# Performance work log

Measured on AMD Instinct MI355X. Metric: run time of the kernel, lower is better.

## Reference

```python
import jax, jax.numpy as jnp
import numpy as np

B, SEQ, DIM = 32, 512, 1024
DEPTH, HEADS, DHEAD = 6, 8, 64
INNER = HEADS * DHEAD  # 512
NLAT, MAXSEQ = 64, 512
EPS = 1e-5


def setup_inputs() -> dict:
    key = jax.random.key(0)
    ks = jax.random.split(key, 8)
    return {
        "x": jax.random.normal(ks[0], (B, SEQ, DIM), dtype=jnp.float32),
        "attention_mask": jax.random.randint(ks[1], (B, SEQ), 0, 2, dtype=jnp.int32),
        "latents": jax.random.normal(ks[2], (NLAT, DIM), dtype=jnp.float32),
        "media_pos_emb": jax.random.normal(ks[3], (MAXSEQ, DIM), dtype=jnp.float32),
        "ln_media_g": jnp.ones((DEPTH, DIM), jnp.float32),
        "ln_media_b": jnp.zeros((DEPTH, DIM), jnp.float32),
        "ln_lat_g": jnp.ones((DEPTH, DIM), jnp.float32),
        "ln_lat_b": jnp.zeros((DEPTH, DIM), jnp.float32),
        "Wq": jax.random.normal(ks[4], (DEPTH, DIM, INNER), dtype=jnp.float32) * 0.02,
        "Wkv": jax.random.normal(ks[5], (DEPTH, DIM, 2 * INNER), dtype=jnp.float32) * 0.02,
        "Wout": jax.random.normal(ks[6], (DEPTH, INNER, DIM), dtype=jnp.float32) * 0.02,
        "final_g": jnp.ones((DIM,), jnp.float32),
        "final_b": jnp.zeros((DIM,), jnp.float32),
    }


def _layer_norm(x, g, b):
    mu = jnp.mean(x, axis=-1, keepdims=True)
    var = jnp.mean(jnp.square(x - mu), axis=-1, keepdims=True)
    return (x - mu) * jax.lax.rsqrt(var + EPS) * g + b


def _heads(t):
    # b n (h d) -> b h n d
    b, n, _ = t.shape
    return t.reshape(b, n, HEADS, DHEAD).transpose(0, 2, 1, 3)


def reference(x, attention_mask, latents, media_pos_emb, ln_media_g, ln_media_b,
              ln_lat_g, ln_lat_b, Wq, Wkv, Wout, final_g, final_b):
    b, seq, _ = x.shape
    x = x + media_pos_emb[None, :seq, :]
    lat = jnp.broadcast_to(latents[None], (b, NLAT, DIM))
    scale = DHEAD ** -0.5
    # key mask over [latents ++ media]: latent keys never masked; 1 == masked
    key_mask = jnp.concatenate(
        [jnp.zeros((b, NLAT), attention_mask.dtype), attention_mask], axis=1)
    masked = (key_mask == 1)[:, None, None, :]  # b 1 1 j
    for l in range(DEPTH):
        xm = _layer_norm(x, ln_media_g[l], ln_media_b[l])
        ln = _layer_norm(lat, ln_lat_g[l], ln_lat_b[l])
        q = _heads(ln @ Wq[l])                      # b h i d
        kv = jnp.concatenate([ln, xm], axis=1) @ Wkv[l]
        k, v = jnp.split(kv, 2, axis=-1)
        k, v = _heads(k), _heads(v)                 # b h j d
        sim = jnp.einsum('bhid,bhjd->bhij', q * scale, k)
        sim = jnp.where(masked, -jnp.inf, sim)
        attn = jax.nn.softmax(sim, axis=-1)
        out = jnp.einsum('bhij,bhjd->bhid', attn, v)
        out = out.transpose(0, 2, 1, 3).reshape(b, NLAT, INNER)
        lat = lat + out @ Wout[l]
    return _layer_norm(lat, final_g, final_b)
```

## Files before the change

### kernel.cpp

```cpp
#include <hip/hip_runtime.h>
#include <cstdint>


#define DEVINL __device__ __forceinline__

typedef __attribute__((ext_vector_type(8))) short short8_t;
typedef __attribute__((ext_vector_type(4))) float f32x4;

DEVINL ushort f2bf(float f) {
  union { float f; uint32_t u; } c; c.f = f;
  uint32_t u = c.u;
  u += ((u >> 16) & 1u) + 0x7fffu;
  return (ushort)(u >> 16);
}
DEVINL float bf2f(ushort u) {
  union { uint32_t u; float f; } c; c.u = ((uint32_t)u) << 16;
  return c.f;
}
DEVINL f32x4 mfma16(short8_t a, short8_t b, f32x4 c) {
  return __builtin_amdgcn_mfma_f32_16x16x32_bf16(a, b, c, 0, 0, 0);
}
DEVINL void gld16(ushort* lds, const ushort* g) {
  __builtin_amdgcn_global_load_lds(
      (const __attribute__((address_space(1))) void*)g,
      (__attribute__((address_space(3))) void*)lds, 16, 0, 0);
}

__global__ __launch_bounds__(512, 2) void k_gemm256m(const ushort* __restrict__ A,
    const ushort* __restrict__ Bt, const float* __restrict__ bias,
    ushort* __restrict__ Kb, ushort* __restrict__ Vt) {
  extern __shared__ char lds[];
  constexpr int K = 1024, NT = 16;
  int tid = threadIdx.x, lane = tid & 63, w = tid >> 6;
  int wm = w >> 2, wn = w & 3;
  int fr = lane & 15;
  int fkb = (lane >> 4) << 4;
  int xorv = (fr & 7) << 4;
  int bid = blockIdx.x;
  int xcd = bid & 7, ii = bid >> 3;
  int m0 = (xcd * 8 + (ii >> 2)) * 256;
  int n0 = (ii & 3) * 256;
  int srow = w * 8 + (lane >> 3);
  int sce = ((lane & 7) ^ (lane >> 3)) << 3;
  const ushort* Ag = A + (size_t)(m0 + srow) * K + sce;
  const ushort* Bg = Bt + (size_t)(n0 + srow) * K + sce;
  f32x4 acc[8][4] = {};

  auto stA = [&](int t, int h) {
    ushort* d = (ushort*)(lds + (t % 3) * 32768 + h * 16384 + w * 1024);
    const ushort* s = Ag + (size_t)(h * 128) * K + t * 64;
    gld16(d, s);
    gld16((ushort*)((char*)d + 8192), s + (size_t)64 * K);
  };
  auto stB = [&](int t, int h) {
    ushort* d = (ushort*)(lds + 98304 + (t & 1) * 32768 + h * 16384 + w * 1024);
    const ushort* s = Bg + (size_t)(h * 128) * K + t * 64;
    gld16(d, s);
    gld16((ushort*)((char*)d + 8192), s + (size_t)64 * K);
  };
  stA(0, 0); stA(0, 1); stB(0, 0); stB(0, 1); stA(1, 0); stA(1, 1);

#define RD_AFR(DST, MQ)                                                        \
  _Pragma("unroll") for (int m2 = 0; m2 < 2; ++m2)                             \
    _Pragma("unroll") for (int kh = 0; kh < 2; ++kh)                           \
      DST[m2][kh] = *(const short8_t*)(ab +                                    \
          ((wm * 128 + (MQ + m2) * 16 + fr) << 7) + ((kh * 64 + fkb) ^ xorv));

#define CLUSTER(MQ, AFR)                                                       \
  __builtin_amdgcn_s_setprio(1);                                               \
  _Pragma("unroll") for (int kh = 0; kh < 2; ++kh)                             \
    _Pragma("unroll") for (int m2 = 0; m2 < 2; ++m2)                           \
      _Pragma("unroll") for (int nt = 0; nt < 4; ++nt)                         \
        acc[MQ + m2][nt] = mfma16(AFR[m2][kh], bfr[nt][kh], acc[MQ + m2][nt]); \
  __builtin_amdgcn_s_setprio(0);                                               \
  __builtin_amdgcn_s_barrier();

  for (int t = 0; t < NT; ++t) {
    const char* ab = lds + (t % 3) * 32768;
    const char* bb = lds + 98304 + (t & 1) * 32768;
    short8_t bfr[4][2], afrX[2][2], afrY[2][2];
    if (t + 1 < NT) asm volatile("s_waitcnt vmcnt(4)" ::: "memory");
    else            asm volatile("s_waitcnt vmcnt(0)" ::: "memory");
    __builtin_amdgcn_s_barrier();
#pragma unroll
    for (int nt = 0; nt < 4; ++nt)
#pragma unroll
      for (int kh = 0; kh < 2; ++kh)
        bfr[nt][kh] = *(const short8_t*)(bb +
            ((wn * 64 + nt * 16 + fr) << 7) + ((kh * 64 + fkb) ^ xorv));
    RD_AFR(afrX, 0);
    if (t + 1 < NT) stB(t + 1, 0);
    RD_AFR(afrY, 2);
    CLUSTER(0, afrX);
    if (t + 1 < NT) stB(t + 1, 1);
    RD_AFR(afrX, 4);
    CLUSTER(2, afrY);
    if (t + 2 < NT) stA(t + 2, 0);
    RD_AFR(afrY, 6);
    CLUSTER(4, afrX);
    if (t + 2 < NT) stA(t + 2, 1);
    CLUSTER(6, afrY);
  }
#undef RD_AFR
#undef CLUSTER

  __syncthreads();
  ushort* Cl = (ushort*)lds;
  constexpr int CLS = 264;
  bool isV = (n0 >= 512);
#pragma unroll
  for (int mt = 0; mt < 8; ++mt)
#pragma unroll
    for (int nt = 0; nt < 4; ++nt)
#pragma unroll
      for (int r = 0; r < 4; ++r) {
        int rl = wm * 128 + mt * 16 + ((lane >> 4) << 2) + r;
        int cl = wn * 64 + nt * 16 + fr;
        ushort v = f2bf(acc[mt][nt][r] + bias[n0 + cl]);
        if (!isV) Cl[rl * CLS + cl] = v;
        else      Cl[cl * CLS + rl] = v;
      }
  __syncthreads();
  int b_ = m0 >> 9;
  int jb = 64 + (m0 & 511);
#pragma unroll
  for (int q2 = 0; q2 < 16; ++q2) {
    int task = tid + q2 * 512;
    int rr2 = task >> 5, c8 = task & 31;
    short8_t vv = *(const short8_t*)&Cl[rr2 * CLS + c8 * 8];
    if (!isV)
      *(short8_t*)&Kb[((size_t)(b_ * 576 + jb + rr2) << 9) + n0 + c8 * 8] = vv;
    else
      *(short8_t*)&Vt[(size_t)(b_ * 512 + (n0 - 512) + rr2) * 576 + jb + c8 * 8] = vv;
  }
}

__global__ __launch_bounds__(512) void k_attn(const ushort* __restrict__ Q,
    const ushort* __restrict__ Kb, const ushort* __restrict__ Vt,
    const int* __restrict__ amask, ushort* __restrict__ AO) {
  extern __shared__ char alds[];
  ushort* sim = (ushort*)alds;
  char* stg = alds + 74752;
  int bh = blockIdx.x;
  int h = bh & 7, b = bh >> 3;
  int tid = threadIdx.x, lane = tid & 63, w = tid >> 6;
  int rg = w >> 1, ch = w & 1;
  int fr = lane & 15;
  int fkb = (lane >> 4) << 4;
  int csrc8 = ((lane & 7) ^ (lane >> 3)) << 3;
  short8_t aq0, aq1;
  {
    int qi = rg * 16 + fr;
    const ushort* qp = Q + ((size_t)(b * 64 + qi) << 9) + h * 64 + ((lane >> 4) << 3);
    aq0 = *(const short8_t*)qp;
    aq1 = *(const short8_t*)(qp + 32);
  }
  unsigned mbits = 0;
#pragma unroll
  for (int c = 1; c < 9; ++c)
    if (amask[b * 512 + (c - 1) * 64 + lane]) mbits |= (1u << c);

  auto stageK = [&](int it, int buf) {
#pragma unroll
    for (int g = 0; g < 3; ++g) {
      int sr = w * 24 + g * 8 + (lane >> 3);
      ushort* d = (ushort*)(stg + buf * 24576 + (w * 24 + g * 8) * 128);
      gld16(d, Kb + ((size_t)(b * 576 + it * 192 + sr) << 9) + h * 64 + csrc8);
    }
  };
  auto stageV = [&](int it, int buf) {
#pragma unroll
    for (int g = 0; g < 3; ++g) {
      int sr = w * 8 + (lane >> 3);
      ushort* d = (ushort*)(stg + buf * 24576 + g * 8192 + w * 8 * 128);
      gld16(d, Vt + (size_t)(b * 512 + h * 64 + sr) * 576 + it * 192 + g * 64 + csrc8);
    }
  };

  stageK(0, 0);
  for (int it = 0; it < 3; ++it) {
    int buf = it & 1;
    __builtin_amdgcn_s_barrier();
    if (it + 1 < 3) {
      stageK(it + 1, buf ^ 1);
      asm volatile("s_waitcnt vmcnt(3)" ::: "memory");
    } else {
      asm volatile("s_waitcnt vmcnt(0)" ::: "memory");
    }
    __builtin_amdgcn_s_barrier();
    const char* kb_ = stg + buf * 24576;
#pragma unroll
    for (int ct = 0; ct < 6; ++ct) {
      int row_l = ch * 96 + ct * 16 + fr;
      const char* base = kb_ + row_l * 128;
      int sw = (row_l & 7) << 4;
      short8_t k0 = *(const short8_t*)(base + (fkb ^ sw));
      short8_t k1 = *(const short8_t*)(base + ((64 + fkb) ^ sw));
      f32x4 s4 = {};
      s4 = mfma16(aq0, k0, s4);
      s4 = mfma16(aq1, k1, s4);
#pragma unroll
      for (int r = 0; r < 4; ++r)
        sim[(rg * 16 + ((lane >> 4) << 2) + r) * 584 +
            it * 192 + ch * 96 + ct * 16 + fr] = f2bf(s4[r]);
    }
  }
  __syncthreads();
  for (int rr = 0; rr < 8; ++rr) {
    int row = w * 8 + rr;
    float vals[9];
    float m = -3.0e38f;
#pragma unroll
    for (int c = 0; c < 9; ++c) {
      float v = bf2f(sim[row * 584 + c * 64 + lane]);
      vals[c] = v;
      if (!((mbits >> c) & 1)) m = fmaxf(m, v);
    }
#pragma unroll
    for (int off = 32; off; off >>= 1) m = fmaxf(m, __shfl_xor(m, off));
    float ssum = 0.f;
    float p[9];
#pragma unroll
    for (int c = 0; c < 9; ++c) {
      p[c] = ((mbits >> c) & 1) ? 0.f : __expf(vals[c] - m);
      ssum += p[c];
    }
#pragma unroll
    for (int off = 32; off; off >>= 1) ssum += __shfl_xor(ssum, off);
    float inv = 1.0f / ssum;
#pragma unroll
    for (int c = 0; c < 9; ++c)
      sim[row * 584 + c * 64 + lane] = f2bf(p[c] * inv);
  }
  __syncthreads();
  f32x4 oacc[2] = {};
  stageV(0, 0);
  for (int it = 0; it < 3; ++it) {
    int buf = it & 1;
    __builtin_amdgcn_s_barrier();
    if (it + 1 < 3) {
      stageV(it + 1, buf ^ 1);
      asm volatile("s_waitcnt vmcnt(3)" ::: "memory");
    } else {
      asm volatile("s_waitcnt vmcnt(0)" ::: "memory");
    }
    __builtin_amdgcn_s_barrier();
#pragma unroll
    for (int g = 0; g < 3; ++g) {
      const char* vb_ = stg + buf * 24576 + g * 8192;
      const ushort* srow_ = &sim[(rg * 16 + fr) * 584 + it * 192 + g * 64];
      short8_t pa0 = *(const short8_t*)(srow_ + ((lane >> 4) << 3));
      short8_t pa1 = *(const short8_t*)(srow_ + 32 + ((lane >> 4) << 3));
#pragma unroll
      for (int dt = 0; dt < 2; ++dt) {
        int row_l = ch * 32 + dt * 16 + fr;
        const char* base = vb_ + row_l * 128;
        int sw = (row_l & 7) << 4;
        short8_t v0 = *(const short8_t*)(base + (fkb ^ sw));
        short8_t v1 = *(const short8_t*)(base + ((64 + fkb) ^ sw));
        oacc[dt] = mfma16(pa0, v0, oacc[dt]);
        oacc[dt] = mfma16(pa1, v1, oacc[dt]);
      }
    }
  }
#pragma unroll
  for (int dt = 0; dt < 2; ++dt)
#pragma unroll
    for (int r = 0; r < 4; ++r) {
      int i = rg * 16 + ((lane >> 4) << 2) + r;
      int d = ch * 32 + dt * 16 + fr;
      AO[((size_t)(b * 64 + i) << 9) + h * 64 + d] = f2bf(oacc[dt][r]);
    }
}

__global__ __launch_bounds__(256) void k_fold_kv(const float* __restrict__ Wkv,
    const float* __restrict__ lnmg, const float* __restrict__ lnlg,
    const float* __restrict__ lnmb, const float* __restrict__ lnlb,
    ushort* __restrict__ wkvmT, ushort* __restrict__ wlatT,
    float* __restrict__ bkvm, float* __restrict__ blat) {
  __shared__ float tile[32][33];
  __shared__ float pm[8][32], pl[8][32];
  int l = blockIdx.y;
  int c0 = blockIdx.x * 32;
  const float* Wl = Wkv + (size_t)l * 1048576;
  int tx = threadIdx.x & 31, ty = threadIdx.x >> 5;
  float am = 0.f, al = 0.f;
  for (int rt = 0; rt < 32; ++rt) {
    int r0 = rt * 32;
    __syncthreads();
#pragma unroll
    for (int i = 0; i < 4; ++i)
      tile[ty + i * 8][tx] = Wl[(size_t)(r0 + ty + i * 8) * 1024 + c0 + tx];
    __syncthreads();
#pragma unroll
    for (int i = 0; i < 4; ++i) {
      int r = ty * 4 + i;
      float wv = tile[r][tx];
      am += lnmb[l * 1024 + r0 + r] * wv;
      al += lnlb[l * 1024 + r0 + r] * wv;
    }
#pragma unroll
    for (int i = 0; i < 4; ++i) {
      int c = ty + i * 8;
      float wv = tile[tx][c];
      int r = r0 + tx;
      wkvmT[(size_t)l * 1048576 + (size_t)(c0 + c) * 1024 + r] =
          f2bf(wv * lnmg[l * 1024 + r]);
      wlatT[(size_t)l * 1572864 + (size_t)(512 + c0 + c) * 1024 + r] =
          f2bf(wv * lnlg[l * 1024 + r]);
    }
  }
  pm[ty][tx] = am; pl[ty][tx] = al;
  __syncthreads();
  if (ty == 0) {
    float sm = 0.f, sl = 0.f;
#pragma unroll
    for (int k = 0; k < 8; ++k) { sm += pm[k][tx]; sl += pl[k][tx]; }
    bkvm[l * 1024 + c0 + tx] = sm;
    blat[l * 1536 + 512 + c0 + tx] = sl;
  }
}

__global__ __launch_bounds__(256) void k_fold_q(const float* __restrict__ Wq,
    const float* __restrict__ lnlg, const float* __restrict__ lnlb,
    ushort* __restrict__ wlatT, float* __restrict__ blat) {
  __shared__ float tile[32][33];
  __shared__ float pq[8][32];
  int l = blockIdx.y;
  int c0 = blockIdx.x * 32;
  const float* Wl = Wq + (size_t)l * 524288;
  int tx = threadIdx.x & 31, ty = threadIdx.x >> 5;
  float aq = 0.f;
  for (int rt = 0; rt < 32; ++rt) {
    int r0 = rt * 32;
    __syncthreads();
#pragma unroll
    for (int i = 0; i < 4; ++i)
      tile[ty + i * 8][tx] = Wl[(size_t)(r0 + ty + i * 8) * 512 + c0 + tx];
    __syncthreads();
#pragma unroll
    for (int i = 0; i < 4; ++i) {
      int r = ty * 4 + i;
      aq += lnlb[l * 1024 + r0 + r] * tile[r][tx];
    }
#pragma unroll
    for (int i = 0; i < 4; ++i) {
      int c = ty + i * 8;
      float wv = tile[tx][c];
      int r = r0 + tx;
      wlatT[(size_t)l * 1572864 + (size_t)(c0 + c) * 1024 + r] =
          f2bf(wv * lnlg[l * 1024 + r] * 0.125f);
    }
  }
  pq[ty][tx] = aq;
  __syncthreads();
  if (ty == 0) {
    float s = 0.f;
#pragma unroll
    for (int k = 0; k < 8; ++k) s += pq[k][tx];
    blat[l * 1536 + c0 + tx] = s * 0.125f;
  }
}

__global__ __launch_bounds__(256) void k_fold_out(const float* __restrict__ Wout,
    ushort* __restrict__ woutT) {
  __shared__ float tile[32][33];
  int l = blockIdx.z;
  const float* Wl = Wout + (size_t)l * 524288;
  int r0 = blockIdx.y * 32, c0 = blockIdx.x * 32;
  int tx = threadIdx.x & 31, ty = threadIdx.x >> 5;
#pragma unroll
  for (int i = 0; i < 4; ++i)
    tile[ty + i * 8][tx] = Wl[(size_t)(r0 + ty + i * 8) * 1024 + c0 + tx];
  __syncthreads();
#pragma unroll
  for (int i = 0; i < 4; ++i) {
    int jl = ty + i * 8;
    woutT[(size_t)l * 524288 + (size_t)(c0 + jl) * 512 + r0 + tx] = f2bf(tile[tx][jl]);
  }
}

__global__ __launch_bounds__(256) void k_rownorm(const float* __restrict__ in,
    const float* __restrict__ pos, ushort* __restrict__ out) {
  int row = blockIdx.x, t = threadIdx.x;
  float4 v = *(const float4*)(in + (size_t)row * 1024 + t * 4);
  if (pos) {
    float4 p = *(const float4*)(pos + (size_t)(row & 511) * 1024 + t * 4);
    v.x += p.x; v.y += p.y; v.z += p.z; v.w += p.w;
  }
  float s = v.x + v.y + v.z + v.w;
  float q = v.x * v.x + v.y * v.y + v.z * v.z + v.w * v.w;
#pragma unroll
  for (int off = 32; off; off >>= 1) { s += __shfl_xor(s, off); q += __shfl_xor(q, off); }
  __shared__ float rs[4], rq[4];
  if ((t & 63) == 0) { rs[t >> 6] = s; rq[t >> 6] = q; }
  __syncthreads();
  s = rs[0] + rs[1] + rs[2] + rs[3];
  q = rq[0] + rq[1] + rq[2] + rq[3];
  float mean = s * (1.0f / 1024.0f);
  float var = q * (1.0f / 1024.0f) - mean * mean;
  float rstd = rsqrtf(var + 1e-5f);
  ushort4 o;
  o.x = f2bf((v.x - mean) * rstd);
  o.y = f2bf((v.y - mean) * rstd);
  o.z = f2bf((v.z - mean) * rstd);
  o.w = f2bf((v.w - mean) * rstd);
  *(ushort4*)(out + (size_t)row * 1024 + t * 4) = o;
}

__global__ __launch_bounds__(256) void k_finalln(const float* __restrict__ in,
    const float* __restrict__ g, const float* __restrict__ b, float* __restrict__ out) {
  int row = blockIdx.x, t = threadIdx.x;
  float4 v = *(const float4*)(in + (size_t)row * 1024 + t * 4);
  float s = v.x + v.y + v.z + v.w;
  float q = v.x * v.x + v.y * v.y + v.z * v.z + v.w * v.w;
#pragma unroll
  for (int off = 32; off; off >>= 1) { s += __shfl_xor(s, off); q += __shfl_xor(q, off); }
  __shared__ float rs[4], rq[4];
  if ((t & 63) == 0) { rs[t >> 6] = s; rq[t >> 6] = q; }
  __syncthreads();
  s = rs[0] + rs[1] + rs[2] + rs[3];
  q = rq[0] + rq[1] + rq[2] + rq[3];
  float mean = s * (1.0f / 1024.0f);
  float var = q * (1.0f / 1024.0f) - mean * mean;
  float rstd = rsqrtf(var + 1e-5f);
  float4 g4 = *(const float4*)(g + t * 4);
  float4 b4 = *(const float4*)(b + t * 4);
  float4 o;
  o.x = (v.x - mean) * rstd * g4.x + b4.x;
  o.y = (v.y - mean) * rstd * g4.y + b4.y;
  o.z = (v.z - mean) * rstd * g4.z + b4.z;
  o.w = (v.w - mean) * rstd * g4.w + b4.w;
  *(float4*)(out + (size_t)row * 1024 + t * 4) = o;
}

__global__ __launch_bounds__(256) void k_latinit(const float* __restrict__ latents,
                                                 float* __restrict__ lat) {
  int row = blockIdx.x, t = threadIdx.x;
  *(float4*)(lat + (size_t)row * 1024 + t * 4) =
      *(const float4*)(latents + (size_t)(row & 63) * 1024 + t * 4);
}

template <int MODE>
__global__ __launch_bounds__(256) void k_gemm64(const ushort* __restrict__ A,
    const ushort* __restrict__ Bt, const float* __restrict__ bias,
    ushort* __restrict__ o0, ushort* __restrict__ o1, ushort* __restrict__ o2,
    float* __restrict__ of, int N, int K) {
  __shared__ ushort Al[2][64][32];
  __shared__ ushort Bl[2][64][32];
  __shared__ ushort Cl[64][72];
  int tid = threadIdx.x, lane = tid & 63, w = tid >> 6;
  int wr = w >> 1, wc = w & 1;
  int m0 = blockIdx.y * 64, n0 = blockIdx.x * 64;
  f32x4 acc[2][2] = {};
  const ushort* Ag = A + (size_t)(m0 + w * 16 + (lane >> 2)) * K + (lane & 3) * 8;
  const ushort* Bg = Bt + (size_t)(n0 + w * 16 + (lane >> 2)) * K + (lane & 3) * 8;
  int fr = lane & 15, fk = (lane >> 4) << 3;
  int nt = K >> 5;
  gld16(&Al[0][w * 16][0], Ag);
  gld16(&Bl[0][w * 16][0], Bg);
  __syncthreads();
  for (int t = 0; t < nt; ++t) {
    int cur = t & 1;
    if (t + 1 < nt) {
      int k0 = (t + 1) << 5;
      gld16(&Al[cur ^ 1][w * 16][0], Ag + k0);
      gld16(&Bl[cur ^ 1][w * 16][0], Bg + k0);
    }
    short8_t a[2], b[2];
#pragma unroll
    for (int mt = 0; mt < 2; ++mt)
      a[mt] = *(const short8_t*)&Al[cur][wr * 32 + mt * 16 + fr][fk];
#pragma unroll
    for (int nt2 = 0; nt2 < 2; ++nt2)
      b[nt2] = *(const short8_t*)&Bl[cur][wc * 32 + nt2 * 16 + fr][fk];
#pragma unroll
    for (int mt = 0; mt < 2; ++mt)
#pragma unroll
      for (int nt2 = 0; nt2 < 2; ++nt2)
        acc[mt][nt2] = mfma16(a[mt], b[nt2], acc[mt][nt2]);
    __syncthreads();
  }
  if constexpr (MODE == 3) {
    if (n0 >= 1024) {
#pragma unroll
      for (int mt = 0; mt < 2; ++mt)
#pragma unroll
        for (int nt2 = 0; nt2 < 2; ++nt2)
#pragma unroll
          for (int r = 0; r < 4; ++r) {
            int rl = wr * 32 + mt * 16 + ((lane >> 4) << 2) + r;
            int col = wc * 32 + nt2 * 16 + (lane & 15);
            Cl[rl][col] = f2bf(acc[mt][nt2][r] + bias[n0 + col]);
          }
      __syncthreads();
      int b_ = m0 >> 6;
#pragma unroll
      for (int q = 0; q < 2; ++q) {
        int task = tid + q * 256;
        int jg = task & 7, d = task >> 3;
        short8_t vv;
#pragma unroll
        for (int e = 0; e < 8; ++e) vv[e] = (short)Cl[jg * 8 + e][d];
        *(short8_t*)&o2[((size_t)(b_ * 512 + (n0 - 1024) + d)) * 576 + jg * 8] = vv;
      }
      return;
    }
  }
#pragma unroll
  for (int mt = 0; mt < 2; ++mt)
#pragma unroll
    for (int nt2 = 0; nt2 < 2; ++nt2)
#pragma unroll
      for (int r = 0; r < 4; ++r) {
        int row = m0 + wr * 32 + mt * 16 + ((lane >> 4) << 2) + r;
        int col = n0 + wc * 32 + nt2 * 16 + (lane & 15);
        float v = acc[mt][nt2][r] + (bias ? bias[col] : 0.0f);
        if constexpr (MODE == 3) {
          int b_ = row >> 6, ii = row & 63;
          if (col < 512) o0[(size_t)row * 512 + col] = f2bf(v);
          else           o1[(((size_t)(b_ * 576 + ii)) << 9) + (col - 512)] = f2bf(v);
        } else {
          of[(size_t)row * N + col] += v;
        }
      }
}

extern "C" void kernel_launch(void* const* d_in, const int* in_sizes, int n_in,
                              void* d_out, int out_size, void* d_ws, size_t ws_size,
                              hipStream_t stream) {
  const float* x       = (const float*)d_in[0];
  const int*   amask   = (const int*)d_in[1];
  const float* latents = (const float*)d_in[2];
  const float* pos     = (const float*)d_in[3];
  const float* lnmg    = (const float*)d_in[4];
  const float* lnmb    = (const float*)d_in[5];
  const float* lnlg    = (const float*)d_in[6];
  const float* lnlb    = (const float*)d_in[7];
  const float* Wq      = (const float*)d_in[8];
  const float* Wkv     = (const float*)d_in[9];
  const float* Wout    = (const float*)d_in[10];
  const float* fg      = (const float*)d_in[11];
  const float* fb      = (const float*)d_in[12];
  float* out = (float*)d_out;
  char* ws = (char*)d_ws;

  ushort* xhat  = (ushort*)(ws + 0);
  ushort* wkvmT = (ushort*)(ws + 33554432);
  ushort* wlatT = (ushort*)(ws + 46137344);
  ushort* woutT = (ushort*)(ws + 65011712);
  float*  bkvm  = (float*)(ws + 71303168);
  float*  blat  = (float*)(ws + 71327744);
  float*  lat   = (float*)(ws + 71364608);
  ushort* lhat  = (ushort*)(ws + 79753216);
  ushort* qbuf  = (ushort*)(ws + 83947520);
  ushort* Kbuf  = (ushort*)(ws + 86044672);
  ushort* Vt    = (ushort*)(ws + 104919040);
  ushort* aobuf = (ushort*)(ws + 123793408);

  (void)hipFuncSetAttribute((const void*)k_gemm256m,
                            hipFuncAttributeMaxDynamicSharedMemorySize, 163840);
  (void)hipFuncSetAttribute((const void*)k_attn,
                            hipFuncAttributeMaxDynamicSharedMemorySize, 131072);

  dim3 B256(256);
  k_fold_kv<<<dim3(32, 6), B256, 0, stream>>>(Wkv, lnmg, lnlg, lnmb, lnlb,
                                              wkvmT, wlatT, bkvm, blat);
  k_fold_q<<<dim3(16, 6), B256, 0, stream>>>(Wq, lnlg, lnlb, wlatT, blat);
  k_fold_out<<<dim3(32, 16, 6), B256, 0, stream>>>(Wout, woutT);
  k_rownorm<<<16384, B256, 0, stream>>>(x, pos, xhat);
  k_latinit<<<2048, B256, 0, stream>>>(latents, lat);

  for (int l = 0; l < 6; ++l) {
    k_rownorm<<<2048, B256, 0, stream>>>(lat, nullptr, lhat);
    k_gemm64<3><<<dim3(24, 32), B256, 0, stream>>>(
        lhat, wlatT + (size_t)l * 1572864, blat + l * 1536,
        qbuf, Kbuf, Vt, nullptr, 1536, 1024);
    k_gemm256m<<<dim3(256), dim3(512), 163840, stream>>>(
        xhat, wkvmT + (size_t)l * 1048576, bkvm + l * 1024, Kbuf, Vt);
    k_attn<<<dim3(256), dim3(512), 123904, stream>>>(qbuf, Kbuf, Vt, amask, aobuf);
    k_gemm64<2><<<dim3(16, 32), B256, 0, stream>>>(
        aobuf, woutT + (size_t)l * 524288, nullptr,
        nullptr, nullptr, nullptr, lat, 1024, 512);
  }
  k_finalln<<<2048, B256, 0, stream>>>(lat, fg, fb, out);
}
```

Measured before the change: 643.4 us.

## Parallelize weight folding over row tiles and enlarge latent GEMM tiles

The weight-fold kernels now launch one block per 32-row tile instead of looping over all rows serially. Per-tile bias partial sums go to a workspace buffer and a new reduction kernel adds them up. The latent projection and output GEMMs move from 64x64 to 128x128 tiles, with a shared-memory staged epilogue that writes Q, K and transposed V as vectorized stores. This cuts the serial fold latency and raises per-block data reuse, but the larger GEMM tiles launch far fewer blocks (192 and 128), which may underfill the GPU.

```diff
diff --git a/kernel.cpp b/kernel.cpp
--- a/kernel.cpp
+++ b/kernel.cpp
@@ -277,89 +277,93 @@
     const float* __restrict__ lnmg, const float* __restrict__ lnlg,
     const float* __restrict__ lnmb, const float* __restrict__ lnlb,
     ushort* __restrict__ wkvmT, ushort* __restrict__ wlatT,
-    float* __restrict__ bkvm, float* __restrict__ blat) {
+    float* __restrict__ pb) {
   __shared__ float tile[32][33];
   __shared__ float pm[8][32], pl[8][32];
-  int l = blockIdx.y;
-  int c0 = blockIdx.x * 32;
+  int l = blockIdx.z, rt = blockIdx.y;
+  int c0 = blockIdx.x * 32, r0 = rt * 32;
   const float* Wl = Wkv + (size_t)l * 1048576;
   int tx = threadIdx.x & 31, ty = threadIdx.x >> 5;
+#pragma unroll
+  for (int i = 0; i < 4; ++i)
+    tile[ty + i * 8][tx] = Wl[(size_t)(r0 + ty + i * 8) * 1024 + c0 + tx];
+  __syncthreads();
   float am = 0.f, al = 0.f;
-  for (int rt = 0; rt < 32; ++rt) {
-    int r0 = rt * 32;
-    __syncthreads();
-#pragma unroll
-    for (int i = 0; i < 4; ++i)
-      tile[ty + i * 8][tx] = Wl[(size_t)(r0 + ty + i * 8) * 1024 + c0 + tx];
-    __syncthreads();
-#pragma unroll
-    for (int i = 0; i < 4; ++i) {
-      int r = ty * 4 + i;
-      float wv = tile[r][tx];
-      am += lnmb[l * 1024 + r0 + r] * wv;
-      al += lnlb[l * 1024 + r0 + r] * wv;
-    }
-#pragma unroll
-    for (int i = 0; i < 4; ++i) {
-      int c = ty + i * 8;
-      float wv = tile[tx][c];
-      int r = r0 + tx;
-      wkvmT[(size_t)l * 1048576 + (size_t)(c0 + c) * 1024 + r] =
-          f2bf(wv * lnmg[l * 1024 + r]);
-      wlatT[(size_t)l * 1572864 + (size_t)(512 + c0 + c) * 1024 + r] =
-          f2bf(wv * lnlg[l * 1024 + r]);
-    }
+#pragma unroll
+  for (int i = 0; i < 4; ++i) {
+    int r = ty * 4 + i;
+    float wv = tile[r][tx];
+    am += lnmb[l * 1024 + r0 + r] * wv;
+    al += lnlb[l * 1024 + r0 + r] * wv;
   }
   pm[ty][tx] = am; pl[ty][tx] = al;
+#pragma unroll
+  for (int i = 0; i < 4; ++i) {
+    int c = ty + i * 8;
+    float wv = tile[tx][c];
+    int r = r0 + tx;
+    wkvmT[(size_t)l * 1048576 + (size_t)(c0 + c) * 1024 + r] =
+        f2bf(wv * lnmg[l * 1024 + r]);
+    wlatT[(size_t)l * 1572864 + (size_t)(512 + c0 + c) * 1024 + r] =
+        f2bf(wv * lnlg[l * 1024 + r]);
+  }
   __syncthreads();
   if (ty == 0) {
     float sm = 0.f, sl = 0.f;
 #pragma unroll
     for (int k = 0; k < 8; ++k) { sm += pm[k][tx]; sl += pl[k][tx]; }
-    bkvm[l * 1024 + c0 + tx] = sm;
-    blat[l * 1536 + 512 + c0 + tx] = sl;
+    pb[(size_t)(l * 32 + rt) * 2560 + c0 + tx] = sm;
+    pb[(size_t)(l * 32 + rt) * 2560 + 1536 + c0 + tx] = sl;
   }
 }
 
 __global__ __launch_bounds__(256) void k_fold_q(const float* __restrict__ Wq,
     const float* __restrict__ lnlg, const float* __restrict__ lnlb,
-    ushort* __restrict__ wlatT, float* __restrict__ blat) {
+    ushort* __restrict__ wlatT, float* __restrict__ pb) {
   __shared__ float tile[32][33];
   __shared__ float pq[8][32];
-  int l = blockIdx.y;
-  int c0 = blockIdx.x * 32;
+  int l = blockIdx.z, rt = blockIdx.y;
+  int c0 = blockIdx.x * 32, r0 = rt * 32;
   const float* Wl = Wq + (size_t)l * 524288;
   int tx = threadIdx.x & 31, ty = threadIdx.x >> 5;
+#pragma unroll
+  for (int i = 0; i < 4; ++i)
+    tile[ty + i * 8][tx] = Wl[(size_t)(r0 + ty + i * 8) * 512 + c0 + tx];
+  __syncthreads();
   float aq = 0.f;
-  for (int rt = 0; rt < 32; ++rt) {
-    int r0 = rt * 32;
-    __syncthreads();
-#pragma unroll
-    for (int i = 0; i < 4; ++i)
-      tile[ty + i * 8][tx] = Wl[(size_t)(r0 + ty + i * 8) * 512 + c0 + tx];
-    __syncthreads();
-#pragma unroll
-    for (int i = 0; i < 4; ++i) {
-      int r = ty * 4 + i;
-      aq += lnlb[l * 1024 + r0 + r] * tile[r][tx];
-    }
-#pragma unroll
-    for (int i = 0; i < 4; ++i) {
-      int c = ty + i * 8;
-      float wv = tile[tx][c];
-      int r = r0 + tx;
-      wlatT[(size_t)l * 1572864 + (size_t)(c0 + c) * 1024 + r] =
-          f2bf(wv * lnlg[l * 1024 + r] * 0.125f);
-    }
+#pragma unroll
+  for (int i = 0; i < 4; ++i) {
+    int r = ty * 4 + i;
+    aq += lnlb[l * 1024 + r0 + r] * tile[r][tx];
   }
   pq[ty][tx] = aq;
+#pragma unroll
+  for (int i = 0; i < 4; ++i) {
+    int c = ty + i * 8;
+    float wv = tile[tx][c];
+    int r = r0 + tx;
+    wlatT[(size_t)l * 1572864 + (size_t)(c0 + c) * 1024 + r] =
+        f2bf(wv * lnlg[l * 1024 + r] * 0.125f);
+  }
   __syncthreads();
   if (ty == 0) {
     float s = 0.f;
 #pragma unroll
     for (int k = 0; k < 8; ++k) s += pq[k][tx];
-    blat[l * 1536 + c0 + tx] = s * 0.125f;
-  }
+    pb[(size_t)(l * 32 + rt) * 2560 + 1024 + c0 + tx] = s;
+  }
+}
+
+__global__ __launch_bounds__(256) void k_bias_red(const float* __restrict__ pb,
+    float* __restrict__ bkvm, float* __restrict__ blat) {
+  int l = blockIdx.y;
+  int c = blockIdx.x * 256 + threadIdx.x;
+  float s = 0.f;
+  for (int rt = 0; rt < 32; ++rt)
+    s += pb[(size_t)(l * 32 + rt) * 2560 + c];
+  if (c < 1024)       bkvm[l * 1024 + c] = s;
+  else if (c < 1536)  blat[l * 1536 + (c - 1024)] = s * 0.125f;
+  else                blat[l * 1536 + 512 + (c - 1536)] = s;
 }
 
 __global__ __launch_bounds__(256) void k_fold_out(const float* __restrict__ Wout,
@@ -442,88 +446,96 @@
 }
 
 template <int MODE>
-__global__ __launch_bounds__(256) void k_gemm64(const ushort* __restrict__ A,
+__global__ __launch_bounds__(256) void k_g128(const ushort* __restrict__ A,
     const ushort* __restrict__ Bt, const float* __restrict__ bias,
     ushort* __restrict__ o0, ushort* __restrict__ o1, ushort* __restrict__ o2,
     float* __restrict__ of, int N, int K) {
-  __shared__ ushort Al[2][64][32];
-  __shared__ ushort Bl[2][64][32];
-  __shared__ ushort Cl[64][72];
+  __shared__ char pool[34816];
   int tid = threadIdx.x, lane = tid & 63, w = tid >> 6;
   int wr = w >> 1, wc = w & 1;
-  int m0 = blockIdx.y * 64, n0 = blockIdx.x * 64;
-  f32x4 acc[2][2] = {};
-  const ushort* Ag = A + (size_t)(m0 + w * 16 + (lane >> 2)) * K + (lane & 3) * 8;
-  const ushort* Bg = Bt + (size_t)(n0 + w * 16 + (lane >> 2)) * K + (lane & 3) * 8;
+  int m0 = blockIdx.y * 128, n0 = blockIdx.x * 128;
+  f32x4 acc[4][4] = {};
+  const ushort* Ag = A + (size_t)(m0 + w * 32 + (lane >> 2)) * K + (lane & 3) * 8;
+  const ushort* Bg = Bt + (size_t)(n0 + w * 32 + (lane >> 2)) * K + (lane & 3) * 8;
   int fr = lane & 15, fk = (lane >> 4) << 3;
-  int nt = K >> 5;
-  gld16(&Al[0][w * 16][0], Ag);
-  gld16(&Bl[0][w * 16][0], Bg);
-  __syncthreads();
-  for (int t = 0; t < nt; ++t) {
+  int ntk = K >> 5;
+  auto stA = [&](int k0, int cur) {
+    ushort* d = (ushort*)pool + cur * 4096 + w * 1024;
+    gld16(d, Ag + k0);
+    gld16(d + 512, Ag + k0 + (size_t)16 * K);
+  };
+  auto stB = [&](int k0, int cur) {
+    ushort* d = (ushort*)(pool + 16384) + cur * 4096 + w * 1024;
+    gld16(d, Bg + k0);
+    gld16(d + 512, Bg + k0 + (size_t)16 * K);
+  };
+  stA(0, 0); stB(0, 0);
+  __syncthreads();
+  for (int t = 0; t < ntk; ++t) {
     int cur = t & 1;
-    if (t + 1 < nt) {
-      int k0 = (t + 1) << 5;
-      gld16(&Al[cur ^ 1][w * 16][0], Ag + k0);
-      gld16(&Bl[cur ^ 1][w * 16][0], Bg + k0);
-    }
-    short8_t a[2], b[2];
-#pragma unroll
-    for (int mt = 0; mt < 2; ++mt)
-      a[mt] = *(const short8_t*)&Al[cur][wr * 32 + mt * 16 + fr][fk];
-#pragma unroll
-    for (int nt2 = 0; nt2 < 2; ++nt2)
-      b[nt2] = *(const short8_t*)&Bl[cur][wc * 32 + nt2 * 16 + fr][fk];
-#pragma unroll
-    for (int mt = 0; mt < 2; ++mt)
-#pragma unroll
-      for (int nt2 = 0; nt2 < 2; ++nt2)
-        acc[mt][nt2] = mfma16(a[mt], b[nt2], acc[mt][nt2]);
+    if (t + 1 < ntk) { stA((t + 1) << 5, cur ^ 1); stB((t + 1) << 5, cur ^ 1); }
+    const ushort* ab = (ushort*)pool + cur * 4096;
+    const ushort* bb = (ushort*)(pool + 16384) + cur * 4096;
+    short8_t a[4], b[4];
+#pragma unroll
+    for (int mt = 0; mt < 4; ++mt)
+      a[mt] = *(const short8_t*)(ab + (wr * 64 + mt * 16 + fr) * 32 + fk);
+#pragma unroll
+    for (int nt = 0; nt < 4; ++nt)
+      b[nt] = *(const short8_t*)(bb + (wc * 64 + nt * 16 + fr) * 32 + fk);
+#pragma unroll
+    for (int mt = 0; mt < 4; ++mt)
+#pragma unroll
+      for (int nt = 0; nt < 4; ++nt)
+        acc[mt][nt] = mfma16(a[mt], b[nt], acc[mt][nt]);
     __syncthreads();
   }
-  if constexpr (MODE == 3) {
-    if (n0 >= 1024) {
-#pragma unroll
-      for (int mt = 0; mt < 2; ++mt)
-#pragma unroll
-        for (int nt2 = 0; nt2 < 2; ++nt2)
-#pragma unroll
-          for (int r = 0; r < 4; ++r) {
-            int rl = wr * 32 + mt * 16 + ((lane >> 4) << 2) + r;
-            int col = wc * 32 + nt2 * 16 + (lane & 15);
-            Cl[rl][col] = f2bf(acc[mt][nt2][r] + bias[n0 + col]);
-          }
-      __syncthreads();
-      int b_ = m0 >> 6;
-#pragma unroll
-      for (int q = 0; q < 2; ++q) {
-        int task = tid + q * 256;
-        int jg = task & 7, d = task >> 3;
-        short8_t vv;
-#pragma unroll
-        for (int e = 0; e < 8; ++e) vv[e] = (short)Cl[jg * 8 + e][d];
-        *(short8_t*)&o2[((size_t)(b_ * 512 + (n0 - 1024) + d)) * 576 + jg * 8] = vv;
+  if constexpr (MODE == 2) {
+#pragma unroll
+    for (int mt = 0; mt < 4; ++mt)
+#pragma unroll
+      for (int nt = 0; nt < 4; ++nt)
+#pragma unroll
+        for (int r = 0; r < 4; ++r) {
+          int row = m0 + wr * 64 + mt * 16 + ((lane >> 4) << 2) + r;
+          int col = n0 + wc * 64 + nt * 16 + fr;
+          of[(size_t)row * N + col] += acc[mt][nt][r];
+        }
+  } else {
+    ushort* Cl = (ushort*)pool;
+    constexpr int CLS = 136;
+    bool isV = (n0 >= 1024);
+#pragma unroll
+    for (int mt = 0; mt < 4; ++mt)
+#pragma unroll
+      for (int nt = 0; nt < 4; ++nt)
+#pragma unroll
+        for (int r = 0; r < 4; ++r) {
+          int rl = wr * 64 + mt * 16 + ((lane >> 4) << 2) + r;
+          int cl = wc * 64 + nt * 16 + fr;
+          ushort v = f2bf(acc[mt][nt][r] + bias[n0 + cl]);
+          if (!isV) Cl[rl * CLS + cl] = v;
+          else      Cl[cl * CLS + rl] = v;
+        }
+    __syncthreads();
+#pragma unroll
+    for (int q = 0; q < 8; ++q) {
+      int task = tid + q * 256;
+      int rr = task >> 4, ck = task & 15;
+      short8_t vv = *(const short8_t*)&Cl[rr * CLS + ck * 8];
+      if (n0 < 512) {
+        *(short8_t*)&o0[(size_t)(m0 + rr) * 512 + n0 + ck * 8] = vv;
+      } else if (n0 < 1024) {
+        int row = m0 + rr, b_ = row >> 6, i = row & 63;
+        *(short8_t*)&o1[((size_t)(b_ * 576 + i) << 9) + (n0 - 512) + ck * 8] = vv;
+      } else {
+        int dg = n0 - 1024 + rr;
+        int b_ = (m0 >> 6) + (ck >> 3);
+        int i0 = (ck & 7) * 8;
+        *(short8_t*)&o2[((size_t)(b_ * 512 + dg)) * 576 + i0] = vv;
       }
-      return;
-    }
-  }
-#pragma unroll
-  for (int mt = 0; mt < 2; ++mt)
-#pragma unroll
-    for (int nt2 = 0; nt2 < 2; ++nt2)
-#pragma unroll
-      for (int r = 0; r < 4; ++r) {
-        int row = m0 + wr * 32 + mt * 16 + ((lane >> 4) << 2) + r;
-        int col = n0 + wc * 32 + nt2 * 16 + (lane & 15);
-        float v = acc[mt][nt2][r] + (bias ? bias[col] : 0.0f);
-        if constexpr (MODE == 3) {
-          int b_ = row >> 6, ii = row & 63;
-          if (col < 512) o0[(size_t)row * 512 + col] = f2bf(v);
-          else           o1[(((size_t)(b_ * 576 + ii)) << 9) + (col - 512)] = f2bf(v);
-        } else {
-          of[(size_t)row * N + col] += v;
-        }
-      }
+    }
+  }
 }
 
 extern "C" void kernel_launch(void* const* d_in, const int* in_sizes, int n_in,
@@ -557,6 +569,7 @@
   ushort* Kbuf  = (ushort*)(ws + 86044672);
   ushort* Vt    = (ushort*)(ws + 104919040);
   ushort* aobuf = (ushort*)(ws + 123793408);
+  float*  pb    = (float*)(ws + 125890560);
 
   (void)hipFuncSetAttribute((const void*)k_gemm256m,
                             hipFuncAttributeMaxDynamicSharedMemorySize, 163840);
@@ -564,22 +577,23 @@
                             hipFuncAttributeMaxDynamicSharedMemorySize, 131072);
 
   dim3 B256(256);
-  k_fold_kv<<<dim3(32, 6), B256, 0, stream>>>(Wkv, lnmg, lnlg, lnmb, lnlb,
-                                              wkvmT, wlatT, bkvm, blat);
-  k_fold_q<<<dim3(16, 6), B256, 0, stream>>>(Wq, lnlg, lnlb, wlatT, blat);
+  k_fold_kv<<<dim3(32, 32, 6), B256, 0, stream>>>(Wkv, lnmg, lnlg, lnmb, lnlb,
+                                                  wkvmT, wlatT, pb);
+  k_fold_q<<<dim3(16, 32, 6), B256, 0, stream>>>(Wq, lnlg, lnlb, wlatT, pb);
   k_fold_out<<<dim3(32, 16, 6), B256, 0, stream>>>(Wout, woutT);
+  k_bias_red<<<dim3(10, 6), B256, 0, stream>>>(pb, bkvm, blat);
   k_rownorm<<<16384, B256, 0, stream>>>(x, pos, xhat);
   k_latinit<<<2048, B256, 0, stream>>>(latents, lat);
 
   for (int l = 0; l < 6; ++l) {
     k_rownorm<<<2048, B256, 0, stream>>>(lat, nullptr, lhat);
-    k_gemm64<3><<<dim3(24, 32), B256, 0, stream>>>(
+    k_g128<3><<<dim3(12, 16), B256, 0, stream>>>(
         lhat, wlatT + (size_t)l * 1572864, blat + l * 1536,
         qbuf, Kbuf, Vt, nullptr, 1536, 1024);
     k_gemm256m<<<dim3(256), dim3(512), 163840, stream>>>(
         xhat, wkvmT + (size_t)l * 1048576, bkvm + l * 1024, Kbuf, Vt);
     k_attn<<<dim3(256), dim3(512), 123904, stream>>>(qbuf, Kbuf, Vt, amask, aobuf);
-    k_gemm64<2><<<dim3(16, 32), B256, 0, stream>>>(
+    k_g128<2><<<dim3(8, 16), B256, 0, stream>>>(
         aobuf, woutT + (size_t)l * 524288, nullptr,
         nullptr, nullptr, nullptr, lat, 1024, 512);
   }
```

After: 666.5 us. 3.6% more time.

## Split weight-fold kernels over row tiles and prefetch V before softmax

Applied to the files above, without the earlier changes.

The k_fold_kv and k_fold_q kernels previously ran a serial 32-step loop over row tiles in only 192 and 96 blocks. Each block now handles a single 32x32 tile, with partial bias sums written to a scratch buffer that a new k_bias_red kernel reduces. This spreads the weight transpose and fold across many more blocks to fill the GPU, at the cost of one extra launch and a partial-sum buffer. Separately, the attention kernel now issues the first V staging load before the softmax so the load overlaps that work.

```diff
diff --git a/kernel.cpp b/kernel.cpp
--- a/kernel.cpp
+++ b/kernel.cpp
@@ -206,6 +206,7 @@
     }
   }
   __syncthreads();
+  stageV(0, 0);
   for (int rr = 0; rr < 8; ++rr) {
     int row = w * 8 + rr;
     float vals[9];
@@ -234,7 +235,6 @@
   }
   __syncthreads();
   f32x4 oacc[2] = {};
-  stageV(0, 0);
   for (int it = 0; it < 3; ++it) {
     int buf = it & 1;
     __builtin_amdgcn_s_barrier();
@@ -277,89 +277,93 @@
     const float* __restrict__ lnmg, const float* __restrict__ lnlg,
     const float* __restrict__ lnmb, const float* __restrict__ lnlb,
     ushort* __restrict__ wkvmT, ushort* __restrict__ wlatT,
-    float* __restrict__ bkvm, float* __restrict__ blat) {
+    float* __restrict__ pb) {
   __shared__ float tile[32][33];
   __shared__ float pm[8][32], pl[8][32];
-  int l = blockIdx.y;
-  int c0 = blockIdx.x * 32;
+  int l = blockIdx.z, rt = blockIdx.y;
+  int c0 = blockIdx.x * 32, r0 = rt * 32;
   const float* Wl = Wkv + (size_t)l * 1048576;
   int tx = threadIdx.x & 31, ty = threadIdx.x >> 5;
+#pragma unroll
+  for (int i = 0; i < 4; ++i)
+    tile[ty + i * 8][tx] = Wl[(size_t)(r0 + ty + i * 8) * 1024 + c0 + tx];
+  __syncthreads();
   float am = 0.f, al = 0.f;
-  for (int rt = 0; rt < 32; ++rt) {
-    int r0 = rt * 32;
-    __syncthreads();
-#pragma unroll
-    for (int i = 0; i < 4; ++i)
-      tile[ty + i * 8][tx] = Wl[(size_t)(r0 + ty + i * 8) * 1024 + c0 + tx];
-    __syncthreads();
-#pragma unroll
-    for (int i = 0; i < 4; ++i) {
-      int r = ty * 4 + i;
-      float wv = tile[r][tx];
-      am += lnmb[l * 1024 + r0 + r] * wv;
-      al += lnlb[l * 1024 + r0 + r] * wv;
-    }
-#pragma unroll
-    for (int i = 0; i < 4; ++i) {
-      int c = ty + i * 8;
-      float wv = tile[tx][c];
-      int r = r0 + tx;
-      wkvmT[(size_t)l * 1048576 + (size_t)(c0 + c) * 1024 + r] =
-          f2bf(wv * lnmg[l * 1024 + r]);
-      wlatT[(size_t)l * 1572864 + (size_t)(512 + c0 + c) * 1024 + r] =
-          f2bf(wv * lnlg[l * 1024 + r]);
-    }
+#pragma unroll
+  for (int i = 0; i < 4; ++i) {
+    int r = ty * 4 + i;
+    float wv = tile[r][tx];
+    am += lnmb[l * 1024 + r0 + r] * wv;
+    al += lnlb[l * 1024 + r0 + r] * wv;
   }
   pm[ty][tx] = am; pl[ty][tx] = al;
+#pragma unroll
+  for (int i = 0; i < 4; ++i) {
+    int c = ty + i * 8;
+    float wv = tile[tx][c];
+    int r = r0 + tx;
+    wkvmT[(size_t)l * 1048576 + (size_t)(c0 + c) * 1024 + r] =
+        f2bf(wv * lnmg[l * 1024 + r]);
+    wlatT[(size_t)l * 1572864 + (size_t)(512 + c0 + c) * 1024 + r] =
+        f2bf(wv * lnlg[l * 1024 + r]);
+  }
   __syncthreads();
   if (ty == 0) {
     float sm = 0.f, sl = 0.f;
 #pragma unroll
     for (int k = 0; k < 8; ++k) { sm += pm[k][tx]; sl += pl[k][tx]; }
-    bkvm[l * 1024 + c0 + tx] = sm;
-    blat[l * 1536 + 512 + c0 + tx] = sl;
+    pb[(size_t)(l * 32 + rt) * 2560 + c0 + tx] = sm;
+    pb[(size_t)(l * 32 + rt) * 2560 + 1536 + c0 + tx] = sl;
   }
 }
 
 __global__ __launch_bounds__(256) void k_fold_q(const float* __restrict__ Wq,
     const float* __restrict__ lnlg, const float* __restrict__ lnlb,
-    ushort* __restrict__ wlatT, float* __restrict__ blat) {
+    ushort* __restrict__ wlatT, float* __restrict__ pb) {
   __shared__ float tile[32][33];
   __shared__ float pq[8][32];
-  int l = blockIdx.y;
-  int c0 = blockIdx.x * 32;
+  int l = blockIdx.z, rt = blockIdx.y;
+  int c0 = blockIdx.x * 32, r0 = rt * 32;
   const float* Wl = Wq + (size_t)l * 524288;
   int tx = threadIdx.x & 31, ty = threadIdx.x >> 5;
+#pragma unroll
+  for (int i = 0; i < 4; ++i)
+    tile[ty + i * 8][tx] = Wl[(size_t)(r0 + ty + i * 8) * 512 + c0 + tx];
+  __syncthreads();
   float aq = 0.f;
-  for (int rt = 0; rt < 32; ++rt) {
-    int r0 = rt * 32;
-    __syncthreads();
-#pragma unroll
-    for (int i = 0; i < 4; ++i)
-      tile[ty + i * 8][tx] = Wl[(size_t)(r0 + ty + i * 8) * 512 + c0 + tx];
-    __syncthreads();
-#pragma unroll
-    for (int i = 0; i < 4; ++i) {
-      int r = ty * 4 + i;
-      aq += lnlb[l * 1024 + r0 + r] * tile[r][tx];
-    }
-#pragma unroll
-    for (int i = 0; i < 4; ++i) {
-      int c = ty + i * 8;
-      float wv = tile[tx][c];
-      int r = r0 + tx;
-      wlatT[(size_t)l * 1572864 + (size_t)(c0 + c) * 1024 + r] =
-          f2bf(wv * lnlg[l * 1024 + r] * 0.125f);
-    }
+#pragma unroll
+  for (int i = 0; i < 4; ++i) {
+    int r = ty * 4 + i;
+    aq += lnlb[l * 1024 + r0 + r] * tile[r][tx];
   }
   pq[ty][tx] = aq;
+#pragma unroll
+  for (int i = 0; i < 4; ++i) {
+    int c = ty + i * 8;
+    float wv = tile[tx][c];
+    int r = r0 + tx;
+    wlatT[(size_t)l * 1572864 + (size_t)(c0 + c) * 1024 + r] =
+        f2bf(wv * lnlg[l * 1024 + r] * 0.125f);
+  }
   __syncthreads();
   if (ty == 0) {
     float s = 0.f;
 #pragma unroll
     for (int k = 0; k < 8; ++k) s += pq[k][tx];
-    blat[l * 1536 + c0 + tx] = s * 0.125f;
-  }
+    pb[(size_t)(l * 32 + rt) * 2560 + 1024 + c0 + tx] = s;
+  }
+}
+
+__global__ __launch_bounds__(256) void k_bias_red(const float* __restrict__ pb,
+    float* __restrict__ bkvm, float* __restrict__ blat) {
+  int l = blockIdx.y;
+  int c = blockIdx.x * 256 + threadIdx.x;
+  float s = 0.f;
+  for (int rt = 0; rt < 32; ++rt)
+    s += pb[(size_t)(l * 32 + rt) * 2560 + c];
+  if (c < 1024)       bkvm[l * 1024 + c] = s;
+  else if (c < 1536)  blat[l * 1536 + (c - 1024)] = s * 0.125f;
+  else                blat[l * 1536 + 512 + (c - 1536)] = s;
 }
 
 __global__ __launch_bounds__(256) void k_fold_out(const float* __restrict__ Wout,
@@ -557,6 +561,7 @@
   ushort* Kbuf  = (ushort*)(ws + 86044672);
   ushort* Vt    = (ushort*)(ws + 104919040);
   ushort* aobuf = (ushort*)(ws + 123793408);
+  float*  pb    = (float*)(ws + 125890560);
 
   (void)hipFuncSetAttribute((const void*)k_gemm256m,
                             hipFuncAttributeMaxDynamicSharedMemorySize, 163840);
@@ -564,10 +569,11 @@
                             hipFuncAttributeMaxDynamicSharedMemorySize, 131072);
 
   dim3 B256(256);
-  k_fold_kv<<<dim3(32, 6), B256, 0, stream>>>(Wkv, lnmg, lnlg, lnmb, lnlb,
-                                              wkvmT, wlatT, bkvm, blat);
-  k_fold_q<<<dim3(16, 6), B256, 0, stream>>>(Wq, lnlg, lnlb, wlatT, blat);
+  k_fold_kv<<<dim3(32, 32, 6), B256, 0, stream>>>(Wkv, lnmg, lnlg, lnmb, lnlb,
+                                                  wkvmT, wlatT, pb);
+  k_fold_q<<<dim3(16, 32, 6), B256, 0, stream>>>(Wq, lnlg, lnlb, wlatT, pb);
   k_fold_out<<<dim3(32, 16, 6), B256, 0, stream>>>(Wout, woutT);
+  k_bias_red<<<dim3(10, 6), B256, 0, stream>>>(pb, bkvm, blat);
   k_rownorm<<<16384, B256, 0, stream>>>(x, pos, xhat);
   k_latinit<<<2048, B256, 0, stream>>>(latents, lat);
 
```

Result: faster. 596.6 us (median of 2 runs) (-7.3%).
